# Optimization experiments

Measured on AMD Instinct MI355X. Metric: run time of the kernel, lower is better.

The kernel has to match this reference:

```python
import jax, jax.numpy as jnp
import numpy as np

N_NODES = 100000
N_EDGES = 600000
IN_DIM = 128
HID = 128
OUT_DIM = 24
NUM_LAYERS = 3


def setup_inputs() -> dict:
    key = jax.random.key(0)
    ks = jax.random.split(key, 12)
    x = jax.random.normal(ks[0], (N_NODES, IN_DIM), dtype=jnp.float32)
    edge_index = jax.random.randint(ks[1], (2, N_EDGES), 0, N_NODES, dtype=jnp.int32)
    def glorot(k, fan_in, fan_out):
        s = jnp.sqrt(6.0 / (fan_in + fan_out))
        return jax.random.uniform(k, (fan_in, fan_out), jnp.float32, -s, s)
    W0 = glorot(ks[2], IN_DIM, HID)
    b0 = jnp.zeros((HID,), jnp.float32)
    W1 = glorot(ks[3], HID, HID)
    b1 = jnp.zeros((HID,), jnp.float32)
    W2 = glorot(ks[4], HID, HID)
    b2 = jnp.zeros((HID,), jnp.float32)
    lin_w = glorot(ks[5], HID, OUT_DIM)
    lin_b = jnp.zeros((OUT_DIM,), jnp.float32)
    return {"x": x, "edge_index": edge_index, "W0": W0, "b0": b0,
            "W1": W1, "b1": b1, "W2": W2, "b2": b2,
            "lin_w": lin_w, "lin_b": lin_b}


def _gcn_norm(edge_index, n_nodes):
    # PyG GCNConv default: add self-loops, symmetric normalization D^-1/2 (A+I) D^-1/2
    loops = jnp.arange(n_nodes, dtype=edge_index.dtype)
    row = jnp.concatenate([edge_index[0], loops])  # source nodes (x_j)
    col = jnp.concatenate([edge_index[1], loops])  # target nodes (aggregation)
    deg = jax.ops.segment_sum(jnp.ones_like(col, dtype=jnp.float32), col,
                              num_segments=n_nodes)
    dinv = jnp.where(deg > 0, jax.lax.rsqrt(deg), 0.0)
    norm = dinv[row] * dinv[col]  # [E + N]
    return row, col, norm


def _gcn_conv(x, W, b, row, col, norm, n_nodes):
    h = x @ W                             # linear first (PyG order)
    msg = h[row] * norm[:, None]          # gather + normalize
    agg = jax.ops.segment_sum(msg, col, num_segments=n_nodes)  # scatter-add
    return agg + b


def reference(x, edge_index, W0, b0, W1, b1, W2, b2, lin_w, lin_b):
    n = x.shape[0]
    row, col, norm = _gcn_norm(edge_index, n)
    for W, b in ((W0, b0), (W1, b1), (W2, b2)):
        x = jax.nn.elu(_gcn_conv(x, W, b, row, col, norm, n))
        # dropout p=0.1 is identity in eval mode
    pooled = jnp.mean(x, axis=0)          # global_mean_pool, single graph
    out = pooled @ lin_w + lin_b          # [24]
    return out
```

## Files before the change

### kernel.cpp

```cpp
#include <hip/hip_runtime.h>
#include <math.h>

#define NN 100000
#define NE 600000
#define DIM 128
#define PBLK 2048
#define GT 1563
#define CNTB 2344
#define CAP 40

typedef __attribute__((ext_vector_type(8))) short short8;
typedef __attribute__((ext_vector_type(4))) float floatx4;

static __device__ __forceinline__ unsigned short f2bf(float f) {
    union { float f; unsigned u; } v; v.f = f;
    unsigned r = v.u + 0x7fffu + ((v.u >> 16) & 1u);
    return (unsigned short)(r >> 16);
}
static __device__ __forceinline__ float bflo(unsigned int p) {
    union { unsigned u; float f; } v; v.u = p << 16; return v.f;
}
static __device__ __forceinline__ float bfhi(unsigned int p) {
    union { unsigned u; float f; } v; v.u = p & 0xffff0000u; return v.f;
}

template <bool A_IS_F32>
static __device__ void gemm_tile(const void* __restrict__ Ain,
                                 const unsigned short* __restrict__ Wp,
                                 unsigned short* __restrict__ H, int n, int tb) {
    __shared__ __align__(16) unsigned short As[64][136];
    const int t = threadIdx.x;
    const int wid = t >> 6, lane = t & 63;
    const int wy = wid & 1, wx = wid >> 1;
    const int base = tb * 64;

    short8 Bf[4][4];
    {
        const short8* wp8 = (const short8*)Wp;
#pragma unroll
        for (int tt = 0; tt < 4; ++tt)
#pragma unroll
            for (int kk = 0; kk < 4; ++kk)
                Bf[tt][kk] = wp8[(((wx * 4 + tt) * 4 + kk) * 64) + lane];
    }

    if constexpr (A_IS_F32) {
        const float* A = (const float*)Ain;
#pragma unroll
        for (int it = 0; it < 8; ++it) {
            int idx = it * 256 + t;
            int row = idx >> 5, seg = idx & 31;
            int r = base + row;
            float4 v = make_float4(0.f, 0.f, 0.f, 0.f);
            if (r < n) v = ((const float4*)(A + (size_t)r * DIM))[seg];
            ushort4 o;
            o.x = f2bf(v.x); o.y = f2bf(v.y); o.z = f2bf(v.z); o.w = f2bf(v.w);
            *((ushort4*)&As[row][seg * 4]) = o;
        }
    } else {
        const unsigned short* A = (const unsigned short*)Ain;
#pragma unroll
        for (int it = 0; it < 4; ++it) {
            int idx = it * 256 + t;
            int row = idx >> 4, seg = idx & 15;
            int r = base + row;
            uint4 v = make_uint4(0, 0, 0, 0);
            if (r < n) v = ((const uint4*)(A + (size_t)r * DIM))[seg];
            *((uint4*)&As[row][seg * 8]) = v;
        }
    }
    __syncthreads();

    floatx4 acc[2][4];
#pragma unroll
    for (int rs = 0; rs < 2; ++rs)
#pragma unroll
        for (int tt = 0; tt < 4; ++tt) acc[rs][tt] = (floatx4){0.f, 0.f, 0.f, 0.f};

    const int m = lane & 15, q = lane >> 4;
#pragma unroll
    for (int rs = 0; rs < 2; ++rs) {
        const int rbase = wy * 32 + rs * 16 + m;
        short8 Af[4];
#pragma unroll
        for (int kk = 0; kk < 4; ++kk)
            Af[kk] = *((const short8*)&As[rbase][kk * 32 + q * 8]);
#pragma unroll
        for (int kk = 0; kk < 4; ++kk)
#pragma unroll
            for (int tt = 0; tt < 4; ++tt)
                acc[rs][tt] = __builtin_amdgcn_mfma_f32_16x16x32_bf16(Af[kk], Bf[tt][kk],
                                                                     acc[rs][tt], 0, 0, 0);
    }
    __syncthreads();

#pragma unroll
    for (int rs = 0; rs < 2; ++rs)
#pragma unroll
        for (int tt = 0; tt < 4; ++tt) {
            const int col = wx * 64 + tt * 16 + m;
            const int rowb = wy * 32 + rs * 16 + q * 4;
#pragma unroll
            for (int i = 0; i < 4; ++i)
                As[rowb + i][col] = f2bf(acc[rs][tt][i]);
        }
    __syncthreads();
#pragma unroll
    for (int it = 0; it < 4; ++it) {
        int idx = it * 256 + t;
        int row = idx >> 4, seg = idx & 15;
        int r = base + row;
        if (r < n)
            ((uint4*)(H + (size_t)r * DIM))[seg] = *((const uint4*)&As[row][seg * 8]);
    }
}

__global__ __launch_bounds__(256) void k_init(int* __restrict__ deg,
                                              const float* __restrict__ W0,
                                              const float* __restrict__ W1,
                                              const float* __restrict__ W2,
                                              unsigned short* __restrict__ Wp) {
    const int bid = blockIdx.x, t = threadIdx.x;
    if (bid < 99) {
        const int base = bid * 1024 + t * 4;
#pragma unroll
        for (int i = 0; i < 4; ++i)
            if (base + i < NN) deg[base + i] = 0;
    } else {
        const int wb = bid - 99;
        const int which = wb >> 6;
        const float* W = which == 0 ? W0 : (which == 1 ? W1 : W2);
        unsigned short* dst = Wp + which * 16384;
        int e = (wb & 63) * 256 + t;
        int j  = e & 7;
        int L  = (e >> 3) & 63;
        int kk = (e >> 9) & 3;
        int ct = e >> 11;
        int k = kk * 32 + (L >> 4) * 8 + j;
        int c = ct * 16 + (L & 15);
        dst[e] = f2bf(W[k * DIM + c]);
    }
}

__global__ __launch_bounds__(256) void k_g0all(const float* __restrict__ x,
                                               const unsigned short* __restrict__ Wp,
                                               unsigned short* __restrict__ H,
                                               const int* __restrict__ rows,
                                               const int* __restrict__ cols,
                                               int* __restrict__ deg,
                                               int* __restrict__ ell, int n, int E) {
    if (blockIdx.x < GT) {
        gemm_tile<true>((const void*)x, Wp, H, n, blockIdx.x);
    } else {
        int e = (blockIdx.x - GT) * 256 + threadIdx.x;
        if (e < E) {
            int r = rows[e];
            int c = cols[e];
            int pos = atomicAdd(&deg[c], 1);
            if (pos < CAP) ell[(size_t)c * CAP + pos] = r;
        }
    }
}

__global__ __launch_bounds__(256) void k_aggemm(const unsigned short* __restrict__ Hin,
                                                const int* __restrict__ deg,
                                                const int* __restrict__ ell,
                                                const float* __restrict__ b,
                                                const unsigned short* __restrict__ Wp,
                                                unsigned short* __restrict__ Hout) {
    __shared__ __align__(16) unsigned short As[16][136];
    const int t = threadIdx.x;
    const int wid = t >> 6, lane = t & 63;
    const int qw = lane >> 4, ql = lane & 15;
    const int base = blockIdx.x * 16;
    const int c = base + wid * 4 + qw;

    const int dt = deg[c];
    const int d = dt < CAP ? dt : CAP;
    const int* er = ell + (size_t)c * CAP;
    int4 e4 = make_int4(0, 0, 0, 0);
    if (d > 0) e4 = *(const int4*)er;
    uint4 hv = *(const uint4*)(Hin + (size_t)c * DIM + ql * 8);
    const float4 bb0 = ((const float4*)b)[ql * 2];
    const float4 bb1 = ((const float4*)b)[ql * 2 + 1];
    const float dc = rsqrtf((float)dt + 1.0f);
    float s = dc * dc;
    float a0 = bb0.x + bflo(hv.x) * s;
    float a1 = bb0.y + bfhi(hv.x) * s;
    float a2 = bb0.z + bflo(hv.y) * s;
    float a3 = bb0.w + bfhi(hv.y) * s;
    float a4 = bb1.x + bflo(hv.z) * s;
    float a5 = bb1.y + bfhi(hv.z) * s;
    float a6 = bb1.z + bflo(hv.w) * s;
    float a7 = bb1.w + bfhi(hv.w) * s;
    int kk = 0;
    while (kk < d) {
        const int i0 = e4.x;
        const int i1 = (kk + 1 < d) ? e4.y : i0;
        const int i2 = (kk + 2 < d) ? e4.z : i0;
        const int i3 = (kk + 3 < d) ? e4.w : i0;
        uint4 v0 = *(const uint4*)(Hin + (size_t)i0 * DIM + ql * 8);
        uint4 v1 = *(const uint4*)(Hin + (size_t)i1 * DIM + ql * 8);
        uint4 v2 = *(const uint4*)(Hin + (size_t)i2 * DIM + ql * 8);
        uint4 v3 = *(const uint4*)(Hin + (size_t)i3 * DIM + ql * 8);
        float w0 = rsqrtf((float)deg[i0] + 1.0f) * dc;
        float w1 = (kk + 1 < d) ? rsqrtf((float)deg[i1] + 1.0f) * dc : 0.f;
        float w2 = (kk + 2 < d) ? rsqrtf((float)deg[i2] + 1.0f) * dc : 0.f;
        float w3 = (kk + 3 < d) ? rsqrtf((float)deg[i3] + 1.0f) * dc : 0.f;
        kk += 4;
        if (kk < d) e4 = *(const int4*)(er + kk);
        a0 += bflo(v0.x) * w0 + bflo(v1.x) * w1 + bflo(v2.x) * w2 + bflo(v3.x) * w3;
        a1 += bfhi(v0.x) * w0 + bfhi(v1.x) * w1 + bfhi(v2.x) * w2 + bfhi(v3.x) * w3;
        a2 += bflo(v0.y) * w0 + bflo(v1.y) * w1 + bflo(v2.y) * w2 + bflo(v3.y) * w3;
        a3 += bfhi(v0.y) * w0 + bfhi(v1.y) * w1 + bfhi(v2.y) * w2 + bfhi(v3.y) * w3;
        a4 += bflo(v0.z) * w0 + bflo(v1.z) * w1 + bflo(v2.z) * w2 + bflo(v3.z) * w3;
        a5 += bfhi(v0.z) * w0 + bfhi(v1.z) * w1 + bfhi(v2.z) * w2 + bfhi(v3.z) * w3;
        a6 += bflo(v0.w) * w0 + bflo(v1.w) * w1 + bflo(v2.w) * w2 + bflo(v3.w) * w3;
        a7 += bfhi(v0.w) * w0 + bfhi(v1.w) * w1 + bfhi(v2.w) * w2 + bfhi(v3.w) * w3;
    }
    a0 = a0 > 0.f ? a0 : expf(a0) - 1.f;
    a1 = a1 > 0.f ? a1 : expf(a1) - 1.f;
    a2 = a2 > 0.f ? a2 : expf(a2) - 1.f;
    a3 = a3 > 0.f ? a3 : expf(a3) - 1.f;
    a4 = a4 > 0.f ? a4 : expf(a4) - 1.f;
    a5 = a5 > 0.f ? a5 : expf(a5) - 1.f;
    a6 = a6 > 0.f ? a6 : expf(a6) - 1.f;
    a7 = a7 > 0.f ? a7 : expf(a7) - 1.f;
    uint4 outv;
    outv.x = (unsigned int)f2bf(a0) | ((unsigned int)f2bf(a1) << 16);
    outv.y = (unsigned int)f2bf(a2) | ((unsigned int)f2bf(a3) << 16);
    outv.z = (unsigned int)f2bf(a4) | ((unsigned int)f2bf(a5) << 16);
    outv.w = (unsigned int)f2bf(a6) | ((unsigned int)f2bf(a7) << 16);
    *(uint4*)&As[wid * 4 + qw][ql * 8] = outv;
    __syncthreads();

    const int m = lane & 15, q = lane >> 4;
    short8 Af[4];
#pragma unroll
    for (int kb = 0; kb < 4; ++kb)
        Af[kb] = *((const short8*)&As[m][kb * 32 + q * 8]);
    const short8* wp8 = (const short8*)Wp;
    short8 Bf[2][4];
#pragma unroll
    for (int tt = 0; tt < 2; ++tt)
#pragma unroll
        for (int kb = 0; kb < 4; ++kb)
            Bf[tt][kb] = wp8[(((wid * 2 + tt) * 4 + kb) * 64) + lane];
    floatx4 acc[2];
    acc[0] = (floatx4){0.f, 0.f, 0.f, 0.f};
    acc[1] = (floatx4){0.f, 0.f, 0.f, 0.f};
#pragma unroll
    for (int kb = 0; kb < 4; ++kb)
#pragma unroll
        for (int tt = 0; tt < 2; ++tt)
            acc[tt] = __builtin_amdgcn_mfma_f32_16x16x32_bf16(Af[kb], Bf[tt][kb], acc[tt], 0, 0, 0);
    __syncthreads();
#pragma unroll
    for (int tt = 0; tt < 2; ++tt)
#pragma unroll
        for (int i = 0; i < 4; ++i)
            As[q * 4 + i][wid * 32 + tt * 16 + m] = f2bf(acc[tt][i]);
    __syncthreads();
    const int r = base + (t >> 4);
    ((uint4*)(Hout + (size_t)r * DIM))[t & 15] = *(const uint4*)&As[t >> 4][(t & 15) * 8];
}

__global__ __launch_bounds__(256) void k_aggpool2(const unsigned short* __restrict__ H,
                                                  const int* __restrict__ deg,
                                                  const int* __restrict__ ell,
                                                  const float* __restrict__ b,
                                                  float* __restrict__ partials,
                                                  float* __restrict__ out, int n) {
    if (blockIdx.x == 0 && threadIdx.x < 24) out[threadIdx.x] = 0.f;
    const int lane = threadIdx.x & 63;
    const int qw = lane >> 4, ql = lane & 15;
    const int wib = threadIdx.x >> 6;
    int p = (blockIdx.x * blockDim.x + threadIdx.x) >> 6;
    const int np = (gridDim.x * blockDim.x) >> 6;
    const int nquad = (n + 3) >> 2;
    const float4 bb0 = ((const float4*)b)[ql * 2];
    const float4 bb1 = ((const float4*)b)[ql * 2 + 1];
    float p0 = 0.f, p1 = 0.f, p2 = 0.f, p3 = 0.f, p4 = 0.f, p5 = 0.f, p6 = 0.f, p7 = 0.f;

    for (; p < nquad; p += np) {
        const int c = p * 4 + qw;
        if (c >= n) continue;
        const int dt = deg[c];
        const int d = dt < CAP ? dt : CAP;
        const int* er = ell + (size_t)c * CAP;
        int4 e4 = make_int4(0, 0, 0, 0);
        if (d > 0) e4 = *(const int4*)er;
        uint4 hv = *(const uint4*)(H + (size_t)c * DIM + ql * 8);
        const float dc = rsqrtf((float)dt + 1.0f);
        float s = dc * dc;
        float a0 = bb0.x + bflo(hv.x) * s;
        float a1 = bb0.y + bfhi(hv.x) * s;
        float a2 = bb0.z + bflo(hv.y) * s;
        float a3 = bb0.w + bfhi(hv.y) * s;
        float a4 = bb1.x + bflo(hv.z) * s;
        float a5 = bb1.y + bfhi(hv.z) * s;
        float a6 = bb1.z + bflo(hv.w) * s;
        float a7 = bb1.w + bfhi(hv.w) * s;
        int kk = 0;
        while (kk < d) {
            const int i0 = e4.x;
            const int i1 = (kk + 1 < d) ? e4.y : i0;
            const int i2 = (kk + 2 < d) ? e4.z : i0;
            const int i3 = (kk + 3 < d) ? e4.w : i0;
            uint4 v0 = *(const uint4*)(H + (size_t)i0 * DIM + ql * 8);
            uint4 v1 = *(const uint4*)(H + (size_t)i1 * DIM + ql * 8);
            uint4 v2 = *(const uint4*)(H + (size_t)i2 * DIM + ql * 8);
            uint4 v3 = *(const uint4*)(H + (size_t)i3 * DIM + ql * 8);
            float w0 = rsqrtf((float)deg[i0] + 1.0f) * dc;
            float w1 = (kk + 1 < d) ? rsqrtf((float)deg[i1] + 1.0f) * dc : 0.f;
            float w2 = (kk + 2 < d) ? rsqrtf((float)deg[i2] + 1.0f) * dc : 0.f;
            float w3 = (kk + 3 < d) ? rsqrtf((float)deg[i3] + 1.0f) * dc : 0.f;
            kk += 4;
            if (kk < d) e4 = *(const int4*)(er + kk);
            a0 += bflo(v0.x) * w0 + bflo(v1.x) * w1 + bflo(v2.x) * w2 + bflo(v3.x) * w3;
            a1 += bfhi(v0.x) * w0 + bfhi(v1.x) * w1 + bfhi(v2.x) * w2 + bfhi(v3.x) * w3;
            a2 += bflo(v0.y) * w0 + bflo(v1.y) * w1 + bflo(v2.y) * w2 + bflo(v3.y) * w3;
            a3 += bfhi(v0.y) * w0 + bfhi(v1.y) * w1 + bfhi(v2.y) * w2 + bfhi(v3.y) * w3;
            a4 += bflo(v0.z) * w0 + bflo(v1.z) * w1 + bflo(v2.z) * w2 + bflo(v3.z) * w3;
            a5 += bfhi(v0.z) * w0 + bfhi(v1.z) * w1 + bfhi(v2.z) * w2 + bfhi(v3.z) * w3;
            a6 += bflo(v0.w) * w0 + bflo(v1.w) * w1 + bflo(v2.w) * w2 + bflo(v3.w) * w3;
            a7 += bfhi(v0.w) * w0 + bfhi(v1.w) * w1 + bfhi(v2.w) * w2 + bfhi(v3.w) * w3;
        }
        p0 += a0 > 0.f ? a0 : expf(a0) - 1.f;
        p1 += a1 > 0.f ? a1 : expf(a1) - 1.f;
        p2 += a2 > 0.f ? a2 : expf(a2) - 1.f;
        p3 += a3 > 0.f ? a3 : expf(a3) - 1.f;
        p4 += a4 > 0.f ? a4 : expf(a4) - 1.f;
        p5 += a5 > 0.f ? a5 : expf(a5) - 1.f;
        p6 += a6 > 0.f ? a6 : expf(a6) - 1.f;
        p7 += a7 > 0.f ? a7 : expf(a7) - 1.f;
    }

    __shared__ float ps[16][DIM];
    *(float4*)&ps[wib * 4 + qw][ql * 8] = make_float4(p0, p1, p2, p3);
    *(float4*)&ps[wib * 4 + qw][ql * 8 + 4] = make_float4(p4, p5, p6, p7);
    __syncthreads();
    const int t = threadIdx.x;
    if (t < DIM) {
        float v = 0.f;
#pragma unroll
        for (int w = 0; w < 16; ++w) v += ps[w][t];
        partials[(size_t)t * PBLK + blockIdx.x] = v;
    }
}

__global__ __launch_bounds__(256) void k_pool2final(const float* __restrict__ partials,
                                                    const float* __restrict__ lw,
                                                    const float* __restrict__ lb,
                                                    float* __restrict__ out) {
    const int d = blockIdx.x;
    const float4* row = (const float4*)(partials + (size_t)d * PBLK);
    float acc = 0.f;
#pragma unroll
    for (int i = 0; i < PBLK / 4 / 256; ++i) {
        float4 v = row[i * 256 + threadIdx.x];
        acc += v.x + v.y + v.z + v.w;
    }
#pragma unroll
    for (int off = 32; off; off >>= 1) acc += __shfl_down(acc, off, 64);
    __shared__ float wsum[4];
    if ((threadIdx.x & 63) == 0) wsum[threadIdx.x >> 6] = acc;
    __syncthreads();
    if (threadIdx.x < 24) {
        float pooled_d = wsum[0] + wsum[1] + wsum[2] + wsum[3];
        float contrib = pooled_d * lw[d * 24 + threadIdx.x] * (1.0f / (float)NN);
        if (d == 0) contrib += lb[threadIdx.x];
        atomicAdd(&out[threadIdx.x], contrib);
    }
}

extern "C" void kernel_launch(void* const* d_in, const int* in_sizes, int n_in,
                              void* d_out, int out_size, void* d_ws, size_t ws_size,
                              hipStream_t stream) {
    const float* x  = (const float*)d_in[0];
    const int*   ei = (const int*)d_in[1];
    const float* W0 = (const float*)d_in[2];
    const float* b0 = (const float*)d_in[3];
    const float* W1 = (const float*)d_in[4];
    const float* b1 = (const float*)d_in[5];
    const float* W2 = (const float*)d_in[6];
    const float* b2 = (const float*)d_in[7];
    const float* lw = (const float*)d_in[8];
    const float* lb = (const float*)d_in[9];
    float* out = (float*)d_out;

    const int N = NN, E = NE;
    const int* rows = ei;
    const int* cols = ei + E;

    char* ws = (char*)d_ws;
    unsigned short* H   = (unsigned short*)ws;
    unsigned short* H2  = (unsigned short*)(ws + 25600000);
    int*   deg = (int*)(ws + 51200000);
    int*   ell = (int*)(ws + 51600000);
    unsigned short* Wp = (unsigned short*)(ws + 67600000);
    float* partials = (float*)(ws + 67698432);

    const int fused_grid = N / 16;

    k_init<<<291, 256, 0, stream>>>(deg, W0, W1, W2, Wp);
    k_g0all<<<GT + CNTB, 256, 0, stream>>>(x, Wp, H, rows, cols, deg, ell, N, E);

    k_aggemm<<<fused_grid, 256, 0, stream>>>(H, deg, ell, b0, Wp + 16384, H2);
    k_aggemm<<<fused_grid, 256, 0, stream>>>(H2, deg, ell, b1, Wp + 32768, H);
    k_aggpool2<<<PBLK, 256, 0, stream>>>(H, deg, ell, b2, partials, out, N);

    k_pool2final<<<DIM, 256, 0, stream>>>(partials, lw, lb, out);
}
```

Before: 266.6 us.

## Pre-scale features by source inverse-sqrt degree to drop per-edge degree gathers

Folds the source-side D^-1/2 factor into each layer's GEMM output, so the aggregation loop sums plain gathered rows and applies the destination factor once per node. This removes the per-edge deg[] gather and rsqrt from the hot loop. Padding lanes now point at a zeroed sentinel row at index NN, so no masking weights are needed. The cost is that the first GEMM can no longer overlap with edge counting: it needs final degrees, so it becomes a separate kernel launched after the fill kernel, adding a serialization point.

```diff
diff --git a/kernel.cpp b/kernel.cpp
--- a/kernel.cpp
+++ b/kernel.cpp
@@ -24,110 +24,41 @@
     union { unsigned u; float f; } v; v.u = p & 0xffff0000u; return v.f;
 }
 
-template <bool A_IS_F32>
-static __device__ void gemm_tile(const void* __restrict__ Ain,
-                                 const unsigned short* __restrict__ Wp,
-                                 unsigned short* __restrict__ H, int n, int tb) {
-    __shared__ __align__(16) unsigned short As[64][136];
-    const int t = threadIdx.x;
-    const int wid = t >> 6, lane = t & 63;
-    const int wy = wid & 1, wx = wid >> 1;
-    const int base = tb * 64;
-
-    short8 Bf[4][4];
-    {
-        const short8* wp8 = (const short8*)Wp;
-#pragma unroll
-        for (int tt = 0; tt < 4; ++tt)
-#pragma unroll
-            for (int kk = 0; kk < 4; ++kk)
-                Bf[tt][kk] = wp8[(((wx * 4 + tt) * 4 + kk) * 64) + lane];
-    }
-
-    if constexpr (A_IS_F32) {
-        const float* A = (const float*)Ain;
-#pragma unroll
-        for (int it = 0; it < 8; ++it) {
-            int idx = it * 256 + t;
-            int row = idx >> 5, seg = idx & 31;
-            int r = base + row;
-            float4 v = make_float4(0.f, 0.f, 0.f, 0.f);
-            if (r < n) v = ((const float4*)(A + (size_t)r * DIM))[seg];
-            ushort4 o;
-            o.x = f2bf(v.x); o.y = f2bf(v.y); o.z = f2bf(v.z); o.w = f2bf(v.w);
-            *((ushort4*)&As[row][seg * 4]) = o;
-        }
+__global__ __launch_bounds__(256) void k_init(int* __restrict__ deg,
+                                              unsigned short* __restrict__ H,
+                                              unsigned short* __restrict__ H2) {
+    const int bid = blockIdx.x, t = threadIdx.x;
+    if (bid < 99) {
+        const int base = bid * 1024 + t * 4;
+#pragma unroll
+        for (int i = 0; i < 4; ++i)
+            if (base + i < NN) deg[base + i] = 0;
+    } else if (bid == 99) {
+        if (t < 16) ((uint4*)(H + (size_t)NN * DIM))[t] = make_uint4(0, 0, 0, 0);
     } else {
-        const unsigned short* A = (const unsigned short*)Ain;
-#pragma unroll
-        for (int it = 0; it < 4; ++it) {
-            int idx = it * 256 + t;
-            int row = idx >> 4, seg = idx & 15;
-            int r = base + row;
-            uint4 v = make_uint4(0, 0, 0, 0);
-            if (r < n) v = ((const uint4*)(A + (size_t)r * DIM))[seg];
-            *((uint4*)&As[row][seg * 8]) = v;
-        }
-    }
-    __syncthreads();
-
-    floatx4 acc[2][4];
-#pragma unroll
-    for (int rs = 0; rs < 2; ++rs)
-#pragma unroll
-        for (int tt = 0; tt < 4; ++tt) acc[rs][tt] = (floatx4){0.f, 0.f, 0.f, 0.f};
-
-    const int m = lane & 15, q = lane >> 4;
-#pragma unroll
-    for (int rs = 0; rs < 2; ++rs) {
-        const int rbase = wy * 32 + rs * 16 + m;
-        short8 Af[4];
-#pragma unroll
-        for (int kk = 0; kk < 4; ++kk)
-            Af[kk] = *((const short8*)&As[rbase][kk * 32 + q * 8]);
-#pragma unroll
-        for (int kk = 0; kk < 4; ++kk)
-#pragma unroll
-            for (int tt = 0; tt < 4; ++tt)
-                acc[rs][tt] = __builtin_amdgcn_mfma_f32_16x16x32_bf16(Af[kk], Bf[tt][kk],
-                                                                     acc[rs][tt], 0, 0, 0);
-    }
-    __syncthreads();
-
-#pragma unroll
-    for (int rs = 0; rs < 2; ++rs)
-#pragma unroll
-        for (int tt = 0; tt < 4; ++tt) {
-            const int col = wx * 64 + tt * 16 + m;
-            const int rowb = wy * 32 + rs * 16 + q * 4;
-#pragma unroll
-            for (int i = 0; i < 4; ++i)
-                As[rowb + i][col] = f2bf(acc[rs][tt][i]);
-        }
-    __syncthreads();
-#pragma unroll
-    for (int it = 0; it < 4; ++it) {
-        int idx = it * 256 + t;
-        int row = idx >> 4, seg = idx & 15;
-        int r = base + row;
-        if (r < n)
-            ((uint4*)(H + (size_t)r * DIM))[seg] = *((const uint4*)&As[row][seg * 8]);
-    }
-}
-
-__global__ __launch_bounds__(256) void k_init(int* __restrict__ deg,
+        if (t < 16) ((uint4*)(H2 + (size_t)NN * DIM))[t] = make_uint4(0, 0, 0, 0);
+    }
+}
+
+__global__ __launch_bounds__(256) void k_fill(const int* __restrict__ rows,
+                                              const int* __restrict__ cols,
+                                              int* __restrict__ deg,
+                                              int* __restrict__ ell,
                                               const float* __restrict__ W0,
                                               const float* __restrict__ W1,
                                               const float* __restrict__ W2,
-                                              unsigned short* __restrict__ Wp) {
-    const int bid = blockIdx.x, t = threadIdx.x;
-    if (bid < 99) {
-        const int base = bid * 1024 + t * 4;
-#pragma unroll
-        for (int i = 0; i < 4; ++i)
-            if (base + i < NN) deg[base + i] = 0;
+                                              unsigned short* __restrict__ Wp, int E) {
+    const int t = threadIdx.x;
+    if (blockIdx.x < CNTB) {
+        int e = blockIdx.x * 256 + t;
+        if (e < E) {
+            int r = rows[e];
+            int c = cols[e];
+            int pos = atomicAdd(&deg[c], 1);
+            if (pos < CAP) ell[(size_t)c * CAP + pos] = r;
+        }
     } else {
-        const int wb = bid - 99;
+        const int wb = blockIdx.x - CNTB;
         const int which = wb >> 6;
         const float* W = which == 0 ? W0 : (which == 1 ? W1 : W2);
         unsigned short* dst = Wp + which * 16384;
@@ -142,23 +73,85 @@
     }
 }
 
-__global__ __launch_bounds__(256) void k_g0all(const float* __restrict__ x,
-                                               const unsigned short* __restrict__ Wp,
-                                               unsigned short* __restrict__ H,
-                                               const int* __restrict__ rows,
-                                               const int* __restrict__ cols,
-                                               int* __restrict__ deg,
-                                               int* __restrict__ ell, int n, int E) {
-    if (blockIdx.x < GT) {
-        gemm_tile<true>((const void*)x, Wp, H, n, blockIdx.x);
-    } else {
-        int e = (blockIdx.x - GT) * 256 + threadIdx.x;
-        if (e < E) {
-            int r = rows[e];
-            int c = cols[e];
-            int pos = atomicAdd(&deg[c], 1);
-            if (pos < CAP) ell[(size_t)c * CAP + pos] = r;
+__global__ __launch_bounds__(256) void k_g0(const float* __restrict__ x,
+                                            const int* __restrict__ deg,
+                                            const unsigned short* __restrict__ Wp,
+                                            unsigned short* __restrict__ H, int n) {
+    __shared__ __align__(16) unsigned short As[64][136];
+    const int t = threadIdx.x;
+    const int wid = t >> 6, lane = t & 63;
+    const int wy = wid & 1, wx = wid >> 1;
+    const int base = blockIdx.x * 64;
+
+    short8 Bf[4][4];
+    {
+        const short8* wp8 = (const short8*)Wp;
+#pragma unroll
+        for (int tt = 0; tt < 4; ++tt)
+#pragma unroll
+            for (int kk = 0; kk < 4; ++kk)
+                Bf[tt][kk] = wp8[(((wx * 4 + tt) * 4 + kk) * 64) + lane];
+    }
+
+#pragma unroll
+    for (int it = 0; it < 8; ++it) {
+        int idx = it * 256 + t;
+        int row = idx >> 5, seg = idx & 31;
+        int r = base + row;
+        float4 v = make_float4(0.f, 0.f, 0.f, 0.f);
+        float ds = 0.f;
+        if (r < n) {
+            v = ((const float4*)(x + (size_t)r * DIM))[seg];
+            ds = rsqrtf((float)deg[r] + 1.0f);
         }
+        ushort4 o;
+        o.x = f2bf(v.x * ds); o.y = f2bf(v.y * ds);
+        o.z = f2bf(v.z * ds); o.w = f2bf(v.w * ds);
+        *((ushort4*)&As[row][seg * 4]) = o;
+    }
+    __syncthreads();
+
+    floatx4 acc[2][4];
+#pragma unroll
+    for (int rs = 0; rs < 2; ++rs)
+#pragma unroll
+        for (int tt = 0; tt < 4; ++tt) acc[rs][tt] = (floatx4){0.f, 0.f, 0.f, 0.f};
+
+    const int m = lane & 15, q = lane >> 4;
+#pragma unroll
+    for (int rs = 0; rs < 2; ++rs) {
+        const int rbase = wy * 32 + rs * 16 + m;
+        short8 Af[4];
+#pragma unroll
+        for (int kk = 0; kk < 4; ++kk)
+            Af[kk] = *((const short8*)&As[rbase][kk * 32 + q * 8]);
+#pragma unroll
+        for (int kk = 0; kk < 4; ++kk)
+#pragma unroll
+            for (int tt = 0; tt < 4; ++tt)
+                acc[rs][tt] = __builtin_amdgcn_mfma_f32_16x16x32_bf16(Af[kk], Bf[tt][kk],
+                                                                     acc[rs][tt], 0, 0, 0);
+    }
+    __syncthreads();
+
+#pragma unroll
+    for (int rs = 0; rs < 2; ++rs)
+#pragma unroll
+        for (int tt = 0; tt < 4; ++tt) {
+            const int col = wx * 64 + tt * 16 + m;
+            const int rowb = wy * 32 + rs * 16 + q * 4;
+#pragma unroll
+            for (int i = 0; i < 4; ++i)
+                As[rowb + i][col] = f2bf(acc[rs][tt][i]);
+        }
+    __syncthreads();
+#pragma unroll
+    for (int it = 0; it < 4; ++it) {
+        int idx = it * 256 + t;
+        int row = idx >> 4, seg = idx & 15;
+        int r = base + row;
+        if (r < n)
+            ((uint4*)(H + (size_t)r * DIM))[seg] = *((const uint4*)&As[row][seg * 8]);
     }
 }
 
@@ -178,46 +171,45 @@
     const int dt = deg[c];
     const int d = dt < CAP ? dt : CAP;
     const int* er = ell + (size_t)c * CAP;
-    int4 e4 = make_int4(0, 0, 0, 0);
+    int4 e4 = make_int4(NN, NN, NN, NN);
     if (d > 0) e4 = *(const int4*)er;
     uint4 hv = *(const uint4*)(Hin + (size_t)c * DIM + ql * 8);
     const float4 bb0 = ((const float4*)b)[ql * 2];
     const float4 bb1 = ((const float4*)b)[ql * 2 + 1];
-    const float dc = rsqrtf((float)dt + 1.0f);
-    float s = dc * dc;
-    float a0 = bb0.x + bflo(hv.x) * s;
-    float a1 = bb0.y + bfhi(hv.x) * s;
-    float a2 = bb0.z + bflo(hv.y) * s;
-    float a3 = bb0.w + bfhi(hv.y) * s;
-    float a4 = bb1.x + bflo(hv.z) * s;
-    float a5 = bb1.y + bfhi(hv.z) * s;
-    float a6 = bb1.z + bflo(hv.w) * s;
-    float a7 = bb1.w + bfhi(hv.w) * s;
+    float a0 = bflo(hv.x), a1 = bfhi(hv.x);
+    float a2 = bflo(hv.y), a3 = bfhi(hv.y);
+    float a4 = bflo(hv.z), a5 = bfhi(hv.z);
+    float a6 = bflo(hv.w), a7 = bfhi(hv.w);
     int kk = 0;
     while (kk < d) {
         const int i0 = e4.x;
-        const int i1 = (kk + 1 < d) ? e4.y : i0;
-        const int i2 = (kk + 2 < d) ? e4.z : i0;
-        const int i3 = (kk + 3 < d) ? e4.w : i0;
+        const int i1 = (kk + 1 < d) ? e4.y : NN;
+        const int i2 = (kk + 2 < d) ? e4.z : NN;
+        const int i3 = (kk + 3 < d) ? e4.w : NN;
         uint4 v0 = *(const uint4*)(Hin + (size_t)i0 * DIM + ql * 8);
         uint4 v1 = *(const uint4*)(Hin + (size_t)i1 * DIM + ql * 8);
         uint4 v2 = *(const uint4*)(Hin + (size_t)i2 * DIM + ql * 8);
         uint4 v3 = *(const uint4*)(Hin + (size_t)i3 * DIM + ql * 8);
-        float w0 = rsqrtf((float)deg[i0] + 1.0f) * dc;
-        float w1 = (kk + 1 < d) ? rsqrtf((float)deg[i1] + 1.0f) * dc : 0.f;
-        float w2 = (kk + 2 < d) ? rsqrtf((float)deg[i2] + 1.0f) * dc : 0.f;
-        float w3 = (kk + 3 < d) ? rsqrtf((float)deg[i3] + 1.0f) * dc : 0.f;
         kk += 4;
         if (kk < d) e4 = *(const int4*)(er + kk);
-        a0 += bflo(v0.x) * w0 + bflo(v1.x) * w1 + bflo(v2.x) * w2 + bflo(v3.x) * w3;
-        a1 += bfhi(v0.x) * w0 + bfhi(v1.x) * w1 + bfhi(v2.x) * w2 + bfhi(v3.x) * w3;
-        a2 += bflo(v0.y) * w0 + bflo(v1.y) * w1 + bflo(v2.y) * w2 + bflo(v3.y) * w3;
-        a3 += bfhi(v0.y) * w0 + bfhi(v1.y) * w1 + bfhi(v2.y) * w2 + bfhi(v3.y) * w3;
-        a4 += bflo(v0.z) * w0 + bflo(v1.z) * w1 + bflo(v2.z) * w2 + bflo(v3.z) * w3;
-        a5 += bfhi(v0.z) * w0 + bfhi(v1.z) * w1 + bfhi(v2.z) * w2 + bfhi(v3.z) * w3;
-        a6 += bflo(v0.w) * w0 + bflo(v1.w) * w1 + bflo(v2.w) * w2 + bflo(v3.w) * w3;
-        a7 += bfhi(v0.w) * w0 + bfhi(v1.w) * w1 + bfhi(v2.w) * w2 + bfhi(v3.w) * w3;
-    }
+        a0 += bflo(v0.x) + bflo(v1.x) + bflo(v2.x) + bflo(v3.x);
+        a1 += bfhi(v0.x) + bfhi(v1.x) + bfhi(v2.x) + bfhi(v3.x);
+        a2 += bflo(v0.y) + bflo(v1.y) + bflo(v2.y) + bflo(v3.y);
+        a3 += bfhi(v0.y) + bfhi(v1.y) + bfhi(v2.y) + bfhi(v3.y);
+        a4 += bflo(v0.z) + bflo(v1.z) + bflo(v2.z) + bflo(v3.z);
+        a5 += bfhi(v0.z) + bfhi(v1.z) + bfhi(v2.z) + bfhi(v3.z);
+        a6 += bflo(v0.w) + bflo(v1.w) + bflo(v2.w) + bflo(v3.w);
+        a7 += bfhi(v0.w) + bfhi(v1.w) + bfhi(v2.w) + bfhi(v3.w);
+    }
+    const float dc = rsqrtf((float)dt + 1.0f);
+    a0 = bb0.x + dc * a0;
+    a1 = bb0.y + dc * a1;
+    a2 = bb0.z + dc * a2;
+    a3 = bb0.w + dc * a3;
+    a4 = bb1.x + dc * a4;
+    a5 = bb1.y + dc * a5;
+    a6 = bb1.z + dc * a6;
+    a7 = bb1.w + dc * a7;
     a0 = a0 > 0.f ? a0 : expf(a0) - 1.f;
     a1 = a1 > 0.f ? a1 : expf(a1) - 1.f;
     a2 = a2 > 0.f ? a2 : expf(a2) - 1.f;
@@ -246,6 +238,9 @@
 #pragma unroll
         for (int kb = 0; kb < 4; ++kb)
             Bf[tt][kb] = wp8[(((wid * 2 + tt) * 4 + kb) * 64) + lane];
+    float dr[4];
+#pragma unroll
+    for (int i = 0; i < 4; ++i) dr[i] = (float)deg[base + q * 4 + i];
     floatx4 acc[2];
     acc[0] = (floatx4){0.f, 0.f, 0.f, 0.f};
     acc[1] = (floatx4){0.f, 0.f, 0.f, 0.f};
@@ -254,12 +249,15 @@
 #pragma unroll
         for (int tt = 0; tt < 2; ++tt)
             acc[tt] = __builtin_amdgcn_mfma_f32_16x16x32_bf16(Af[kb], Bf[tt][kb], acc[tt], 0, 0, 0);
+    float sc[4];
+#pragma unroll
+    for (int i = 0; i < 4; ++i) sc[i] = rsqrtf(dr[i] + 1.0f);
     __syncthreads();
 #pragma unroll
     for (int tt = 0; tt < 2; ++tt)
 #pragma unroll
         for (int i = 0; i < 4; ++i)
-            As[q * 4 + i][wid * 32 + tt * 16 + m] = f2bf(acc[tt][i]);
+            As[q * 4 + i][wid * 32 + tt * 16 + m] = f2bf(acc[tt][i] * sc[i]);
     __syncthreads();
     const int r = base + (t >> 4);
     ((uint4*)(Hout + (size_t)r * DIM))[t & 15] = *(const uint4*)&As[t >> 4][(t & 15) * 8];
@@ -288,44 +286,43 @@
         const int dt = deg[c];
         const int d = dt < CAP ? dt : CAP;
         const int* er = ell + (size_t)c * CAP;
-        int4 e4 = make_int4(0, 0, 0, 0);
+        int4 e4 = make_int4(NN, NN, NN, NN);
         if (d > 0) e4 = *(const int4*)er;
         uint4 hv = *(const uint4*)(H + (size_t)c * DIM + ql * 8);
-        const float dc = rsqrtf((float)dt + 1.0f);
-        float s = dc * dc;
-        float a0 = bb0.x + bflo(hv.x) * s;
-        float a1 = bb0.y + bfhi(hv.x) * s;
-        float a2 = bb0.z + bflo(hv.y) * s;
-        float a3 = bb0.w + bfhi(hv.y) * s;
-        float a4 = bb1.x + bflo(hv.z) * s;
-        float a5 = bb1.y + bfhi(hv.z) * s;
-        float a6 = bb1.z + bflo(hv.w) * s;
-        float a7 = bb1.w + bfhi(hv.w) * s;
+        float a0 = bflo(hv.x), a1 = bfhi(hv.x);
+        float a2 = bflo(hv.y), a3 = bfhi(hv.y);
+        float a4 = bflo(hv.z), a5 = bfhi(hv.z);
+        float a6 = bflo(hv.w), a7 = bfhi(hv.w);
         int kk = 0;
         while (kk < d) {
             const int i0 = e4.x;
-            const int i1 = (kk + 1 < d) ? e4.y : i0;
-            const int i2 = (kk + 2 < d) ? e4.z : i0;
-            const int i3 = (kk + 3 < d) ? e4.w : i0;
+            const int i1 = (kk + 1 < d) ? e4.y : NN;
+            const int i2 = (kk + 2 < d) ? e4.z : NN;
+            const int i3 = (kk + 3 < d) ? e4.w : NN;
             uint4 v0 = *(const uint4*)(H + (size_t)i0 * DIM + ql * 8);
             uint4 v1 = *(const uint4*)(H + (size_t)i1 * DIM + ql * 8);
             uint4 v2 = *(const uint4*)(H + (size_t)i2 * DIM + ql * 8);
             uint4 v3 = *(const uint4*)(H + (size_t)i3 * DIM + ql * 8);
-            float w0 = rsqrtf((float)deg[i0] + 1.0f) * dc;
-            float w1 = (kk + 1 < d) ? rsqrtf((float)deg[i1] + 1.0f) * dc : 0.f;
-            float w2 = (kk + 2 < d) ? rsqrtf((float)deg[i2] + 1.0f) * dc : 0.f;
-            float w3 = (kk + 3 < d) ? rsqrtf((float)deg[i3] + 1.0f) * dc : 0.f;
             kk += 4;
             if (kk < d) e4 = *(const int4*)(er + kk);
-            a0 += bflo(v0.x) * w0 + bflo(v1.x) * w1 + bflo(v2.x) * w2 + bflo(v3.x) * w3;
-            a1 += bfhi(v0.x) * w0 + bfhi(v1.x) * w1 + bfhi(v2.x) * w2 + bfhi(v3.x) * w3;
-            a2 += bflo(v0.y) * w0 + bflo(v1.y) * w1 + bflo(v2.y) * w2 + bflo(v3.y) * w3;
-            a3 += bfhi(v0.y) * w0 + bfhi(v1.y) * w1 + bfhi(v2.y) * w2 + bfhi(v3.y) * w3;
-            a4 += bflo(v0.z) * w0 + bflo(v1.z) * w1 + bflo(v2.z) * w2 + bflo(v3.z) * w3;
-            a5 += bfhi(v0.z) * w0 + bfhi(v1.z) * w1 + bfhi(v2.z) * w2 + bfhi(v3.z) * w3;
-            a6 += bflo(v0.w) * w0 + bflo(v1.w) * w1 + bflo(v2.w) * w2 + bflo(v3.w) * w3;
-            a7 += bfhi(v0.w) * w0 + bfhi(v1.w) * w1 + bfhi(v2.w) * w2 + bfhi(v3.w) * w3;
+            a0 += bflo(v0.x) + bflo(v1.x) + bflo(v2.x) + bflo(v3.x);
+            a1 += bfhi(v0.x) + bfhi(v1.x) + bfhi(v2.x) + bfhi(v3.x);
+            a2 += bflo(v0.y) + bflo(v1.y) + bflo(v2.y) + bflo(v3.y);
+            a3 += bfhi(v0.y) + bfhi(v1.y) + bfhi(v2.y) + bfhi(v3.y);
+            a4 += bflo(v0.z) + bflo(v1.z) + bflo(v2.z) + bflo(v3.z);
+            a5 += bfhi(v0.z) + bfhi(v1.z) + bfhi(v2.z) + bfhi(v3.z);
+            a6 += bflo(v0.w) + bflo(v1.w) + bflo(v2.w) + bflo(v3.w);
+            a7 += bfhi(v0.w) + bfhi(v1.w) + bfhi(v2.w) + bfhi(v3.w);
         }
+        const float dc = rsqrtf((float)dt + 1.0f);
+        a0 = bb0.x + dc * a0;
+        a1 = bb0.y + dc * a1;
+        a2 = bb0.z + dc * a2;
+        a3 = bb0.w + dc * a3;
+        a4 = bb1.x + dc * a4;
+        a5 = bb1.y + dc * a5;
+        a6 = bb1.z + dc * a6;
+        a7 = bb1.w + dc * a7;
         p0 += a0 > 0.f ? a0 : expf(a0) - 1.f;
         p1 += a1 > 0.f ? a1 : expf(a1) - 1.f;
         p2 += a2 > 0.f ? a2 : expf(a2) - 1.f;
@@ -395,16 +392,17 @@
 
     char* ws = (char*)d_ws;
     unsigned short* H   = (unsigned short*)ws;
-    unsigned short* H2  = (unsigned short*)(ws + 25600000);
-    int*   deg = (int*)(ws + 51200000);
-    int*   ell = (int*)(ws + 51600000);
-    unsigned short* Wp = (unsigned short*)(ws + 67600000);
-    float* partials = (float*)(ws + 67698432);
+    unsigned short* H2  = (unsigned short*)(ws + 25600256);
+    int*   deg = (int*)(ws + 51200512);
+    int*   ell = (int*)(ws + 51600512);
+    unsigned short* Wp = (unsigned short*)(ws + 67600512);
+    float* partials = (float*)(ws + 67698816);
 
     const int fused_grid = N / 16;
 
-    k_init<<<291, 256, 0, stream>>>(deg, W0, W1, W2, Wp);
-    k_g0all<<<GT + CNTB, 256, 0, stream>>>(x, Wp, H, rows, cols, deg, ell, N, E);
+    k_init<<<101, 256, 0, stream>>>(deg, H, H2);
+    k_fill<<<CNTB + 192, 256, 0, stream>>>(rows, cols, deg, ell, W0, W1, W2, Wp, E);
+    k_g0<<<GT, 256, 0, stream>>>(x, deg, Wp, H, N);
 
     k_aggemm<<<fused_grid, 256, 0, stream>>>(H, deg, ell, b0, Wp + 16384, H2);
     k_aggemm<<<fused_grid, 256, 0, stream>>>(H2, deg, ell, b1, Wp + 32768, H);
```

Result: faster. 242.0 us (median of 2 runs) (-9.2%).
